# Optimization experiments

Hardware: AMD Instinct MI355X
Metric: run time of the kernel (lower is better)

Reference implementation:

```python
import jax, jax.numpy as jnp
import numpy as np


def setup_inputs() -> dict:
    key = jax.random.key(0)
    ks = jax.random.split(key, 10)
    B, D_X, D_H, D_S, D_T = 16384, 256, 512, 128, 128
    G = 4 * D_H
    sc = lambda d: 1.0 / np.sqrt(d)
    return {
        "x": jax.random.normal(ks[0], (B, D_X), jnp.float32),
        "h": jax.random.normal(ks[1], (B, D_H), jnp.float32),
        "c": jax.random.normal(ks[2], (B, D_H), jnp.float32),
        "spatial_per_step": jax.random.normal(ks[3], (B, D_S), jnp.float32),
        "temporal_per_step": jax.random.normal(ks[4], (B, D_T), jnp.float32),
        "W_x": jax.random.normal(ks[5], (D_X, G), jnp.float32) * sc(D_X),
        "W_h": jax.random.normal(ks[6], (D_H, G), jnp.float32) * sc(D_H),
        "b_h": jax.random.normal(ks[7], (G,), jnp.float32) * 0.01,
        "W_s": jax.random.normal(ks[8], (D_S, G), jnp.float32) * sc(D_S),
        "W_t": jax.random.normal(ks[9], (D_T, G), jnp.float32) * sc(D_T),
    }


def reference(x, h, c, spatial_per_step, temporal_per_step, W_x, W_h, b_h, W_s, W_t):
    H = W_h.shape[0]  # hidden_size
    # Four gate projections summed (the fusion opportunity): [B, 4H]
    preact = (x @ W_x) + (h @ W_h + b_h) + (spatial_per_step @ W_s) + (temporal_per_step @ W_t)
    i_g = jax.nn.sigmoid(preact[:, 0 * H:1 * H])
    f_g = jax.nn.sigmoid(preact[:, 1 * H:2 * H])
    o_g = jax.nn.sigmoid(preact[:, 2 * H:3 * H])
    c_g = jnp.tanh(preact[:, 3 * H:4 * H])
    c_new = f_g * c + i_g * c_g
    # NOTE: faithful to the source, h = tanh(o * c) (not o * tanh(c))
    h_new = jnp.tanh(o_g * c_new)
    return (h_new, c_new)
```

## Files before the change

kernel.cpp:

```cpp
#include <hip/hip_runtime.h>
#include <hip/hip_bf16.h>
#include <cstdint>

#define B_DIM 16384
#define DX 256
#define DH 512
#define DS 128
#define DT 128
#define KDIM 1024
#define NDIM 2048
#define HOUT 512

typedef __attribute__((ext_vector_type(8))) short short8;
typedef __attribute__((ext_vector_type(4))) float floatx4;

union bf16x8 {
  short8 v;
  __hip_bfloat16 b[8];
};

__device__ __forceinline__ float fast_sigmoid(float x) {
  return 1.f / (1.f + __expf(-x));
}
__device__ __forceinline__ float fast_tanh(float x) {
  float e = __expf(-2.f * x);
  return (1.f - e) / (1.f + e);
}


__global__ __launch_bounds__(256) void pack_A(
    const float* __restrict__ x, const float* __restrict__ h,
    const float* __restrict__ s, const float* __restrict__ t,
    __hip_bfloat16* __restrict__ Ap) {
  int tid = blockIdx.x * 256 + threadIdx.x;
  int r = tid >> 7;
  int k = (tid & 127) * 8;
  const float* p;
  if (k < 768) {
    p = (k < 256) ? (x + (size_t)r * DX + k) : (h + (size_t)r * DH + (k - 256));
  } else {
    p = (k < 896) ? (s + (size_t)r * DS + (k - 768)) : (t + (size_t)r * DT + (k - 896));
  }
  floatx4 v0 = *(const floatx4*)p;
  floatx4 v1 = *(const floatx4*)(p + 4);
  bf16x8 o;
#pragma unroll
  for (int j = 0; j < 4; ++j) {
    o.b[j]     = __float2bfloat16(v0[j]);
    o.b[4 + j] = __float2bfloat16(v1[j]);
  }
  *(short8*)(Ap + (size_t)tid * 8) = o.v;
}

__global__ __launch_bounds__(256) void pack_W(
    const float* __restrict__ Wx, const float* __restrict__ Wh,
    const float* __restrict__ Ws, const float* __restrict__ Wt,
    __hip_bfloat16* __restrict__ Wp) {
  int tid = blockIdx.x * 256 + threadIdx.x;
  int i = tid & 63;
  int tt = (tid >> 6) & 15;
  int tile = tid >> 10;
  int kb = tile & 15, nblk = tile >> 4;
  int sp = tt >> 3, c = tt & 7;
  int nl = c * 16 + (i >> 2);
  int k = kb * 64 + sp * 32 + (i & 3) * 8;
  int wn = nl >> 6, g = (nl >> 4) & 3, hl = nl & 15;
  int col = g * 512 + nblk * 32 + wn * 16 + hl;
  const float* src; int kl;
  if (k < 256)      { src = Wx; kl = k; }
  else if (k < 768) { src = Wh; kl = k - 256; }
  else if (k < 896) { src = Ws; kl = k - 768; }
  else              { src = Wt; kl = k - 896; }
  bf16x8 o;
#pragma unroll
  for (int r = 0; r < 8; ++r)
    o.b[r] = __float2bfloat16(src[(size_t)(kl + r) * NDIM + col]);
  *(short8*)(Wp + (size_t)tid * 8) = o.v;
}

__global__ __launch_bounds__(256, 4) void lstm_gemm(
    const __hip_bfloat16* __restrict__ Ap, const __hip_bfloat16* __restrict__ Wp,
    const float* __restrict__ bh, const float* __restrict__ c_in,
    float* __restrict__ out) {
  __shared__ unsigned short As[128 * 32];
  __shared__ unsigned short Bs[128 * 32];

  const int tid = threadIdx.x;
  const int lane = tid & 63;
  const int wid = tid >> 6;
  const int wm = wid & 1;
  const int wn = wid >> 1;
  const int q = lane >> 4;
  const int fr = lane & 15;
  const int mb = blockIdx.y;
  const int nblk = blockIdx.x;
  const int m0 = mb * 128;

  floatx4 acc[4][4];
#pragma unroll
  for (int i = 0; i < 4; ++i)
#pragma unroll
    for (int j = 0; j < 4; ++j) acc[i][j] = (floatx4)0.f;

  const int arow_in_chunk = lane >> 2;
  const int akoff = (lane & 3) * 8;

  for (int p = 0; p < 32; ++p) {
    const int k0 = p * 32;
    const size_t bbase = ((size_t)((nblk * 16 + (p >> 1)) * 16 + (p & 1) * 8)) * 512;
#pragma unroll
    for (int j = 0; j < 2; ++j) {
      const int chunk = wid * 2 + j;
      __builtin_amdgcn_global_load_lds(
          (const __attribute__((address_space(1))) void*)
              (Ap + (size_t)(m0 + chunk * 16 + arow_in_chunk) * KDIM + k0 + akoff),
          (__attribute__((address_space(3))) void*)&As[chunk * 512], 16, 0, 0);
      __builtin_amdgcn_global_load_lds(
          (const __attribute__((address_space(1))) void*)
              (Wp + bbase + (size_t)chunk * 512 + lane * 8),
          (__attribute__((address_space(3))) void*)&Bs[chunk * 512], 16, 0, 0);
    }
    __syncthreads();

    short8 af[4], bf[4];
#pragma unroll
    for (int i = 0; i < 4; ++i) {
      af[i] = *(const short8*)&As[(wm * 64 + i * 16 + fr) * 32 + q * 8];
      bf[i] = *(const short8*)&Bs[(wn * 64 + i * 16 + fr) * 32 + q * 8];
    }
#pragma unroll
    for (int mi = 0; mi < 4; ++mi)
#pragma unroll
      for (int ni = 0; ni < 4; ++ni)
        acc[mi][ni] = __builtin_amdgcn_mfma_f32_16x16x32_bf16(
            af[mi], bf[ni], acc[mi][ni], 0, 0, 0);
    __syncthreads();
  }

  const int hh = nblk * 32 + wn * 16 + fr;
  float bias[4];
#pragma unroll
  for (int g = 0; g < 4; ++g) bias[g] = bh[g * 512 + hh];

#pragma unroll
  for (int mi = 0; mi < 4; ++mi) {
#pragma unroll
    for (int r = 0; r < 4; ++r) {
      const size_t grow = (size_t)(m0 + wm * 64 + mi * 16 + q * 4 + r);
      const float pi = acc[mi][0][r] + bias[0];
      const float pf = acc[mi][1][r] + bias[1];
      const float po = acc[mi][2][r] + bias[2];
      const float pc = acc[mi][3][r] + bias[3];
      const float ig = fast_sigmoid(pi);
      const float fg = fast_sigmoid(pf);
      const float og = fast_sigmoid(po);
      const float cg = fast_tanh(pc);
      const float cc = fg * c_in[grow * HOUT + hh] + ig * cg;
      out[grow * HOUT + hh] = fast_tanh(og * cc);
      out[(size_t)B_DIM * HOUT + grow * HOUT + hh] = cc;
    }
  }
}

extern "C" void kernel_launch(void* const* d_in, const int* in_sizes, int n_in,
                              void* d_out, int out_size, void* d_ws, size_t ws_size,
                              hipStream_t stream) {
  const float* x  = (const float*)d_in[0];
  const float* h  = (const float*)d_in[1];
  const float* c  = (const float*)d_in[2];
  const float* sp = (const float*)d_in[3];
  const float* tp = (const float*)d_in[4];
  const float* Wx = (const float*)d_in[5];
  const float* Wh = (const float*)d_in[6];
  const float* bh = (const float*)d_in[7];
  const float* Ws = (const float*)d_in[8];
  const float* Wt = (const float*)d_in[9];
  float* out = (float*)d_out;

  __hip_bfloat16* Ap = (__hip_bfloat16*)d_ws;
  __hip_bfloat16* Wp = (__hip_bfloat16*)((char*)d_ws + (size_t)B_DIM * KDIM * 2);

  pack_A<<<dim3(B_DIM * KDIM / 8 / 256), dim3(256), 0, stream>>>(x, h, sp, tp, Ap);
  pack_W<<<dim3(NDIM * KDIM / 8 / 256), dim3(256), 0, stream>>>(Wx, Wh, Ws, Wt, Wp);
  lstm_gemm<<<dim3(NDIM / 128, B_DIM / 128), dim3(256), 0, stream>>>(Ap, Wp, bh, c, out);
}
```

Before: 241.9 us.

## Triple-buffer GEMM LDS loads, swizzle LDS layout, remap blocks, merge pack kernels

The GEMM now prefetches two K-steps ahead into a three-slot LDS ring, with one waitcnt plus barrier per iteration instead of two syncthreads, so global loads overlap the MFMAs. LDS rows are XOR-swizzled to reduce bank conflicts, and the weight pack switches to a plain row-major N×K layout. Blocks are remapped across XCD groups for L2 locality, s_setprio is raised around the MFMA loop, and the two pack kernels are merged into one launch. The larger LDS footprint lowers occupancy to 3 blocks per CU.

```diff
diff --git a/kernel.cpp b/kernel.cpp
--- a/kernel.cpp
+++ b/kernel.cpp
@@ -11,6 +11,9 @@
 #define NDIM 2048
 #define HOUT 512
 
+#define NT 32
+#define SLOT 4096
+
 typedef __attribute__((ext_vector_type(8))) short short8;
 typedef __attribute__((ext_vector_type(4))) float floatx4;
 
@@ -28,62 +31,63 @@
 }
 
 
-__global__ __launch_bounds__(256) void pack_A(
+__global__ __launch_bounds__(256) void pack_AW(
     const float* __restrict__ x, const float* __restrict__ h,
     const float* __restrict__ s, const float* __restrict__ t,
-    __hip_bfloat16* __restrict__ Ap) {
-  int tid = blockIdx.x * 256 + threadIdx.x;
-  int r = tid >> 7;
-  int k = (tid & 127) * 8;
-  const float* p;
-  if (k < 768) {
-    p = (k < 256) ? (x + (size_t)r * DX + k) : (h + (size_t)r * DH + (k - 256));
-  } else {
-    p = (k < 896) ? (s + (size_t)r * DS + (k - 768)) : (t + (size_t)r * DT + (k - 896));
-  }
-  floatx4 v0 = *(const floatx4*)p;
-  floatx4 v1 = *(const floatx4*)(p + 4);
-  bf16x8 o;
-#pragma unroll
-  for (int j = 0; j < 4; ++j) {
-    o.b[j]     = __float2bfloat16(v0[j]);
-    o.b[4 + j] = __float2bfloat16(v1[j]);
-  }
-  *(short8*)(Ap + (size_t)tid * 8) = o.v;
-}
-
-__global__ __launch_bounds__(256) void pack_W(
     const float* __restrict__ Wx, const float* __restrict__ Wh,
     const float* __restrict__ Ws, const float* __restrict__ Wt,
-    __hip_bfloat16* __restrict__ Wp) {
-  int tid = blockIdx.x * 256 + threadIdx.x;
-  int i = tid & 63;
-  int tt = (tid >> 6) & 15;
-  int tile = tid >> 10;
-  int kb = tile & 15, nblk = tile >> 4;
-  int sp = tt >> 3, c = tt & 7;
-  int nl = c * 16 + (i >> 2);
-  int k = kb * 64 + sp * 32 + (i & 3) * 8;
-  int wn = nl >> 6, g = (nl >> 4) & 3, hl = nl & 15;
-  int col = g * 512 + nblk * 32 + wn * 16 + hl;
-  const float* src; int kl;
-  if (k < 256)      { src = Wx; kl = k; }
-  else if (k < 768) { src = Wh; kl = k - 256; }
-  else if (k < 896) { src = Ws; kl = k - 768; }
-  else              { src = Wt; kl = k - 896; }
-  bf16x8 o;
-#pragma unroll
-  for (int r = 0; r < 8; ++r)
-    o.b[r] = __float2bfloat16(src[(size_t)(kl + r) * NDIM + col]);
-  *(short8*)(Wp + (size_t)tid * 8) = o.v;
-}
-
-__global__ __launch_bounds__(256, 4) void lstm_gemm(
+    __hip_bfloat16* __restrict__ Ap, __hip_bfloat16* __restrict__ Wp) {
+  const int bid = blockIdx.x;
+  if (bid < B_DIM * KDIM / 8 / 256) {
+    int tid = bid * 256 + threadIdx.x;
+    int r = tid >> 7;
+    int k = (tid & 127) * 8;
+    const float* p;
+    if (k < 768) {
+      p = (k < 256) ? (x + (size_t)r * DX + k) : (h + (size_t)r * DH + (k - 256));
+    } else {
+      p = (k < 896) ? (s + (size_t)r * DS + (k - 768)) : (t + (size_t)r * DT + (k - 896));
+    }
+    floatx4 v0 = *(const floatx4*)p;
+    floatx4 v1 = *(const floatx4*)(p + 4);
+    bf16x8 o;
+#pragma unroll
+    for (int j = 0; j < 4; ++j) {
+      o.b[j]     = __float2bfloat16(v0[j]);
+      o.b[4 + j] = __float2bfloat16(v1[j]);
+    }
+    *(short8*)(Ap + (size_t)tid * 8) = o.v;
+  } else {
+    int tid = (bid - B_DIM * KDIM / 8 / 256) * 256 + threadIdx.x;
+    int pcol = tid >> 7;
+    int k0 = (tid & 127) * 8;
+    int nblk = pcol >> 7, r7 = pcol & 127;
+    int wn = r7 >> 6, g = (r7 >> 4) & 3, hl = r7 & 15;
+    int col = g * 512 + nblk * 32 + wn * 16 + hl;
+    const float* src; int kl;
+    if (k0 < 256)      { src = Wx; kl = k0; }
+    else if (k0 < 768) { src = Wh; kl = k0 - 256; }
+    else if (k0 < 896) { src = Ws; kl = k0 - 768; }
+    else               { src = Wt; kl = k0 - 896; }
+    bf16x8 o;
+#pragma unroll
+    for (int rr = 0; rr < 8; ++rr)
+      o.b[rr] = __float2bfloat16(src[(size_t)(kl + rr) * NDIM + col]);
+    *(short8*)(Wp + (size_t)tid * 8) = o.v;
+  }
+}
+
+#define GLD(src, dst)                                              \
+  __builtin_amdgcn_global_load_lds(                                \
+      (const __attribute__((address_space(1))) void*)(src),        \
+      (__attribute__((address_space(3))) void*)(dst), 16, 0, 0)
+
+__global__ __launch_bounds__(256, 3) void lstm_gemm(
     const __hip_bfloat16* __restrict__ Ap, const __hip_bfloat16* __restrict__ Wp,
     const float* __restrict__ bh, const float* __restrict__ c_in,
     float* __restrict__ out) {
-  __shared__ unsigned short As[128 * 32];
-  __shared__ unsigned short Bs[128 * 32];
+  __shared__ unsigned short As[3 * SLOT];
+  __shared__ unsigned short Bs[3 * SLOT];
 
   const int tid = threadIdx.x;
   const int lane = tid & 63;
@@ -92,49 +96,79 @@
   const int wn = wid >> 1;
   const int q = lane >> 4;
   const int fr = lane & 15;
-  const int mb = blockIdx.y;
-  const int nblk = blockIdx.x;
+
+  const int bid = blockIdx.x;
+  const int wg = (bid & 7) * 256 + (bid >> 3);
+  const int mb = wg >> 4;
+  const int nblk = wg & 15;
   const int m0 = mb * 128;
 
+  int aOff[4], bOff[4];
+#pragma unroll
+  for (int m = 0; m < 4; ++m) {
+    int row = wm * 64 + m * 16 + fr;
+    aOff[m] = row * 32 + (q ^ ((row >> 1) & 3)) * 8;
+  }
+#pragma unroll
+  for (int n = 0; n < 4; ++n) {
+    int colc = wn * 64 + n * 16 + fr;
+    bOff[n] = colc * 32 + (q ^ ((colc >> 1) & 3)) * 8;
+  }
+
+  const int c0 = wid * 2, c1 = c0 + 1;
+  const int r0 = c0 * 16 + (lane >> 2), r1 = c1 * 16 + (lane >> 2);
+  const int ql = lane & 3;
+  const int q0 = ql ^ ((r0 >> 1) & 3);
+  const int q1 = ql ^ ((r1 >> 1) & 3);
+  const __hip_bfloat16* aP0 = Ap + (size_t)(m0 + r0) * KDIM + q0 * 8;
+  const __hip_bfloat16* aP1 = Ap + (size_t)(m0 + r1) * KDIM + q1 * 8;
+  const __hip_bfloat16* bP0 = Wp + (size_t)(nblk * 128 + r0) * KDIM + q0 * 8;
+  const __hip_bfloat16* bP1 = Wp + (size_t)(nblk * 128 + r1) * KDIM + q1 * 8;
+  const int dA0 = c0 * 512, dA1 = c1 * 512;
+
   floatx4 acc[4][4];
 #pragma unroll
   for (int i = 0; i < 4; ++i)
 #pragma unroll
     for (int j = 0; j < 4; ++j) acc[i][j] = (floatx4)0.f;
 
-  const int arow_in_chunk = lane >> 2;
-  const int akoff = (lane & 3) * 8;
-
-  for (int p = 0; p < 32; ++p) {
-    const int k0 = p * 32;
-    const size_t bbase = ((size_t)((nblk * 16 + (p >> 1)) * 16 + (p & 1) * 8)) * 512;
-#pragma unroll
-    for (int j = 0; j < 2; ++j) {
-      const int chunk = wid * 2 + j;
-      __builtin_amdgcn_global_load_lds(
-          (const __attribute__((address_space(1))) void*)
-              (Ap + (size_t)(m0 + chunk * 16 + arow_in_chunk) * KDIM + k0 + akoff),
-          (__attribute__((address_space(3))) void*)&As[chunk * 512], 16, 0, 0);
-      __builtin_amdgcn_global_load_lds(
-          (const __attribute__((address_space(1))) void*)
-              (Wp + bbase + (size_t)chunk * 512 + lane * 8),
-          (__attribute__((address_space(3))) void*)&Bs[chunk * 512], 16, 0, 0);
-    }
-    __syncthreads();
+  GLD(aP0,      &As[dA0]);        GLD(aP1,      &As[dA1]);
+  GLD(bP0,      &Bs[dA0]);        GLD(bP1,      &Bs[dA1]);
+  GLD(aP0 + 32, &As[SLOT + dA0]); GLD(aP1 + 32, &As[SLOT + dA1]);
+  GLD(bP0 + 32, &Bs[SLOT + dA0]); GLD(bP1 + 32, &Bs[SLOT + dA1]);
+  asm volatile("s_waitcnt vmcnt(4)\n\ts_barrier" ::: "memory");
+
+  int sR = 0;
+  int sS = 2 * SLOT;
+
+  for (int t = 0; t < NT; ++t) {
+    const int ts = (t + 2 < NT) ? (t + 2) : (NT - 1);
+    const int kO = ts * 32;
+
+    GLD(aP0 + kO, &As[sS + dA0]);
+    GLD(aP1 + kO, &As[sS + dA1]);
+    GLD(bP0 + kO, &Bs[sS + dA0]);
+    GLD(bP1 + kO, &Bs[sS + dA1]);
 
     short8 af[4], bf[4];
 #pragma unroll
-    for (int i = 0; i < 4; ++i) {
-      af[i] = *(const short8*)&As[(wm * 64 + i * 16 + fr) * 32 + q * 8];
-      bf[i] = *(const short8*)&Bs[(wn * 64 + i * 16 + fr) * 32 + q * 8];
-    }
+    for (int i = 0; i < 4; ++i) af[i] = *(const short8*)&As[sR + aOff[i]];
+#pragma unroll
+    for (int i = 0; i < 4; ++i) bf[i] = *(const short8*)&Bs[sR + bOff[i]];
+
+    __builtin_amdgcn_s_setprio(1);
 #pragma unroll
     for (int mi = 0; mi < 4; ++mi)
 #pragma unroll
       for (int ni = 0; ni < 4; ++ni)
         acc[mi][ni] = __builtin_amdgcn_mfma_f32_16x16x32_bf16(
             af[mi], bf[ni], acc[mi][ni], 0, 0, 0);
-    __syncthreads();
+    __builtin_amdgcn_s_setprio(0);
+
+    asm volatile("s_waitcnt vmcnt(4)\n\ts_barrier" ::: "memory");
+
+    sR = (sR == 2 * SLOT) ? 0 : sR + SLOT;
+    sS = (sS == 2 * SLOT) ? 0 : sS + SLOT;
   }
 
   const int hh = nblk * 32 + wn * 16 + fr;
@@ -180,7 +214,9 @@
   __hip_bfloat16* Ap = (__hip_bfloat16*)d_ws;
   __hip_bfloat16* Wp = (__hip_bfloat16*)((char*)d_ws + (size_t)B_DIM * KDIM * 2);
 
-  pack_A<<<dim3(B_DIM * KDIM / 8 / 256), dim3(256), 0, stream>>>(x, h, sp, tp, Ap);
-  pack_W<<<dim3(NDIM * KDIM / 8 / 256), dim3(256), 0, stream>>>(Wx, Wh, Ws, Wt, Wp);
-  lstm_gemm<<<dim3(NDIM / 128, B_DIM / 128), dim3(256), 0, stream>>>(Ap, Wp, bh, c, out);
-}
+  const int nblk_A = B_DIM * KDIM / 8 / 256;
+  const int nblk_W = NDIM * KDIM / 8 / 256;
+  pack_AW<<<dim3(nblk_A + nblk_W), dim3(256), 0, stream>>>(
+      x, h, sp, tp, Wx, Wh, Ws, Wt, Ap, Wp);
+  lstm_gemm<<<dim3(2048), dim3(256), 0, stream>>>(Ap, Wp, bh, c, out);
+}
```

New measurement: 263.4 us. 1.09x slower.
